# Performance work log

Measured on AMD Instinct MI355X. Metric: run time of the kernel, lower is better.

Reference implementation:

```python
import jax, jax.numpy as jnp
import numpy as np

EPS = 1e-5


def _lstm(x, W_ih, W_hh, b_ih, b_hh):
    # x: [B, T, in]; torch LSTM gate order i, f, g, o. Returns (last h, last c).
    def step(carry, xt):
        h, c = carry
        z = xt @ W_ih.T + h @ W_hh.T + (b_ih + b_hh)  # [B, 4H]
        i, f, g, o = jnp.split(z, 4, axis=-1)
        c = jax.nn.sigmoid(f) * c + jax.nn.sigmoid(i) * jnp.tanh(g)
        h = jax.nn.sigmoid(o) * jnp.tanh(c)
        return (h, c), None
    h0 = jnp.zeros((x.shape[0], W_hh.shape[1]), x.dtype)
    (h, c), _ = jax.lax.scan(step, (h0, h0), jnp.swapaxes(x, 0, 1))
    return h, c


def _bn_train(x, g, b):
    # BatchNorm1d in training mode: batch stats, biased variance.
    m = x.mean(axis=0)
    v = x.var(axis=0)
    return g * (x - m) * jax.lax.rsqrt(v + EPS) + b


def _forward(agent_traj, neighbours, aW_ih, aW_hh, ab_ih, ab_hh,
             nW_ih, nW_hh, nb_ih, nb_hh, dW_ih, dW_hh, db_ih, db_hh,
             pW, pb, rW, rb, m1W, m1b, g1, be1, m2W, m2b, g2, be2,
             i1W, i1b, ig1, ib1, i2W, i2b, ig2, ib2, segment_ids):
    B = agent_traj.shape[0]
    # relative distance: neighbour last position - owning agent's last position
    rel = neighbours[:, -1, :] - agent_traj[segment_ids, -1, :]          # [N, 2]
    agent_h, agent_c = _lstm(agent_traj, aW_ih, aW_hh, ab_ih, ab_hh)     # [B, 64]
    neigh_h, _ = _lstm(neighbours, nW_ih, nW_hh, nb_ih, nb_hh)           # [N, 64]
    rel_emb = rel @ rW.T + rb                                            # [N, 64]
    x = jnp.concatenate([neigh_h, rel_emb], axis=1)                      # [N, 128]
    x = _bn_train(jax.nn.relu(x @ m1W.T + m1b), g1, be1)                 # [N, 512]
    x = _bn_train(jax.nn.relu(x @ m2W.T + m2b), g2, be2)                 # [N, 1024]
    # per-sample max pooling over each sample's neighbours (zeros if none)
    pooled = jax.ops.segment_max(x, segment_ids, num_segments=B)         # [B, 1024]
    counts = jax.ops.segment_sum(jnp.ones((x.shape[0],), x.dtype), segment_ids, num_segments=B)
    pooled = jnp.where(counts[:, None] > 0, pooled, jnp.zeros((), x.dtype))
    d = jnp.concatenate([pooled, agent_h], axis=1)                       # [B, 1088]
    d = _bn_train(jax.nn.relu(d @ i1W.T + i1b), ig1, ib1)                # [B, 1024]
    d = _bn_train(jax.nn.relu(d @ i2W.T + i2b), ig2, ib2)                # [B, 64]

    def dec_step(carry, _):
        h, c = carry
        z = h @ dW_ih.T + h @ dW_hh.T + (db_ih + db_hh)
        i, f, g, o = jnp.split(z, 4, axis=-1)
        c = jax.nn.sigmoid(f) * c + jax.nn.sigmoid(i) * jnp.tanh(g)
        h = jax.nn.sigmoid(o) * jnp.tanh(c)
        return (h, c), h
    _, hs = jax.lax.scan(dec_step, (d, agent_c), None, length=30)        # [30, B, 64]
    pred = jnp.einsum('tbh,oh->bto', hs, pW) + pb                        # [B, 30, 2]
    return pred


def setup_inputs() -> dict:
    B, T, N, Tn, H = 2048, 20, 32768, 20, 64
    key = jax.random.key(0)
    ki = iter(jax.random.split(key, 40))
    def rn(shape, s=0.1):
        return jax.random.normal(next(ki), shape, dtype=jnp.float32) * s
    inp = dict(
        agent_traj=rn((B, T, 2), 1.0),
        neighbours=rn((N, Tn, 2), 1.0),
        aW_ih=rn((4 * H, 2)), aW_hh=rn((4 * H, H)), ab_ih=rn((4 * H,)), ab_hh=rn((4 * H,)),
        nW_ih=rn((4 * H, 2)), nW_hh=rn((4 * H, H)), nb_ih=rn((4 * H,)), nb_hh=rn((4 * H,)),
        dW_ih=rn((4 * H, H)), dW_hh=rn((4 * H, H)), db_ih=rn((4 * H,)), db_hh=rn((4 * H,)),
        pW=rn((2, H)), pb=rn((2,)),
        rW=rn((H, 2)), rb=rn((H,)),
        m1W=rn((512, 128)), m1b=rn((512,)),
        g1=jnp.ones((512,), jnp.float32), be1=jnp.zeros((512,), jnp.float32),
        m2W=rn((1024, 512)), m2b=rn((1024,)),
        g2=jnp.ones((1024,), jnp.float32), be2=jnp.zeros((1024,), jnp.float32),
        i1W=rn((1024, 1088)), i1b=rn((1024,)),
        ig1=jnp.ones((1024,), jnp.float32), ib1=jnp.zeros((1024,), jnp.float32),
        i2W=rn((H, 1024)), i2b=rn((H,)),
        ig2=jnp.ones((H,), jnp.float32), ib2=jnp.zeros((H,), jnp.float32),
        segment_ids=jnp.sort(jax.random.randint(next(ki), (N,), 0, B)).astype(jnp.int32),
    )
    return inp


def reference(agent_traj, neighbours, aW_ih, aW_hh, ab_ih, ab_hh,
              nW_ih, nW_hh, nb_ih, nb_hh, dW_ih, dW_hh, db_ih, db_hh,
              pW, pb, rW, rb, m1W, m1b, g1, be1, m2W, m2b, g2, be2,
              i1W, i1b, ig1, ib1, i2W, i2b, ig2, ib2, segment_ids):
    return _forward(agent_traj, neighbours, aW_ih, aW_hh, ab_ih, ab_hh,
                    nW_ih, nW_hh, nb_ih, nb_hh, dW_ih, dW_hh, db_ih, db_hh,
                    pW, pb, rW, rb, m1W, m1b, g1, be1, m2W, m2b, g2, be2,
                    i1W, i1b, ig1, ib1, i2W, i2b, ig2, ib2, segment_ids)
```

## Files before the change

kernel.cpp:

```cpp
#include <hip/hip_runtime.h>

#define EPS_BN 1e-5f

typedef __attribute__((ext_vector_type(8))) short short8;
typedef __attribute__((ext_vector_type(4))) float f32x4;

__device__ __forceinline__ float fast_rcp(float x) { return __builtin_amdgcn_rcpf(x); }
__device__ __forceinline__ float sigmoid_f(float x) { return fast_rcp(1.0f + __expf(-x)); }
__device__ __forceinline__ float tanh_f(float x) { return 1.0f - 2.0f * fast_rcp(__expf(2.0f * x) + 1.0f); }

__device__ __forceinline__ unsigned short f2bf(float f) {
    unsigned u = __float_as_uint(f);
    u += 0x7FFFu + ((u >> 16) & 1u);
    return (unsigned short)(u >> 16);
}
__device__ __forceinline__ unsigned pk_bf(float a, float b) {
    return (unsigned)f2bf(a) | ((unsigned)f2bf(b) << 16);
}
__device__ __forceinline__ float bf_hi(float f) {
    return __uint_as_float((unsigned)f2bf(f) << 16);
}

__device__ __forceinline__ void gload16(const unsigned short* g, unsigned short* l) {
    __builtin_amdgcn_global_load_lds(
        (const __attribute__((address_space(1))) unsigned int*)g,
        (__attribute__((address_space(3))) unsigned int*)l,
        16, 0, 0);
}

union AFrag { short e[8]; short8 v; };
union BFrag { uint4 u; short8 v; };

__global__ __launch_bounds__(256) void lstm_mfma(
    const float* __restrict__ xA,
    const float* __restrict__ aW_ih, const float* __restrict__ aW_hh,
    const float* __restrict__ ab_ih, const float* __restrict__ ab_hh,
    float* __restrict__ agent_h, float* __restrict__ agent_c,
    const float* __restrict__ xN,
    const float* __restrict__ nW_ih, const float* __restrict__ nW_hh,
    const float* __restrict__ nb_ih, const float* __restrict__ nb_hh,
    const int* __restrict__ seg, const float* __restrict__ rW,
    const float* __restrict__ rb,
    unsigned short* __restrict__ x0hi, unsigned short* __restrict__ x0lo,
    int nAgentBlk, int T)
{
    __shared__ unsigned h_ex[2][2][32 * 52];

    const bool isA = (blockIdx.x < (unsigned)nAgentBlk);
    const long blk = isA ? blockIdx.x : blockIdx.x - nAgentBlk;
    const float* __restrict__ x     = isA ? xA   : xN;
    const float* __restrict__ W_ih  = isA ? aW_ih : nW_ih;
    const float* __restrict__ W_hh  = isA ? aW_hh : nW_hh;
    const float* __restrict__ b_ih  = isA ? ab_ih : nb_ih;
    const float* __restrict__ b_hh  = isA ? ab_hh : nb_hh;

    const int tid  = threadIdx.x;
    const int w    = tid >> 6;
    const int lane = tid & 63;
    const int s    = lane & 15;
    const int q    = lane >> 4;

    short8 ahi[4][3], alo[4][3];
#pragma unroll
    for (int gt = 0; gt < 4; ++gt) {
        const int n = gt * 64 + w * 16 + s;
#pragma unroll
        for (int kc = 0; kc < 2; ++kc) {
            const float* src = &W_hh[n * 64 + kc * 32 + q * 8];
            float4 v0 = *(const float4*)src;
            float4 v1 = *(const float4*)(src + 4);
            float v[8] = {v0.x, v0.y, v0.z, v0.w, v1.x, v1.y, v1.z, v1.w};
            AFrag a, b;
#pragma unroll
            for (int j = 0; j < 8; ++j) {
                a.e[j] = (short)f2bf(v[j]);
                b.e[j] = (short)f2bf(v[j] - bf_hi(v[j]));
            }
            ahi[gt][kc] = a.v;
            alo[gt][kc] = b.v;
        }
        AFrag a2, b2;
#pragma unroll
        for (int j = 0; j < 8; ++j) { a2.e[j] = 0; b2.e[j] = 0; }
        if (q == 0) {
            const float wi0 = W_ih[n * 2 + 0];
            const float wi1 = W_ih[n * 2 + 1];
            const float bs  = b_ih[n] + b_hh[n];
            a2.e[0] = (short)f2bf(wi0); b2.e[0] = (short)f2bf(wi0 - bf_hi(wi0));
            a2.e[1] = (short)f2bf(wi1); b2.e[1] = (short)f2bf(wi1 - bf_hi(wi1));
            a2.e[2] = (short)f2bf(bs);  b2.e[2] = (short)f2bf(bs  - bf_hi(bs));
        }
        ahi[gt][2] = a2.v;
        alo[gt][2] = b2.v;
    }

    for (int i = tid; i < 2 * 2 * 32 * 52; i += 256) (&h_ex[0][0][0])[i] = 0u;
    __syncthreads();
    if (tid < 32) {
        h_ex[0][0][tid * 52 + 33] = pk_bf(1.0f, 0.0f);
        h_ex[1][0][tid * 52 + 33] = pk_bf(1.0f, 0.0f);
        float2 xv = *(const float2*)&x[(blk * 32 + tid) * (long)(T * 2)];
        h_ex[0][0][tid * 52 + 32] = pk_bf(xv.x, xv.y);
        h_ex[0][1][tid * 52 + 32] = pk_bf(xv.x - bf_hi(xv.x), xv.y - bf_hi(xv.y));
    }
    __syncthreads();

    float creg[2][4] = {{0.f, 0.f, 0.f, 0.f}, {0.f, 0.f, 0.f, 0.f}};

    for (int t = 0; t < T; ++t) {
        const int rb_ = t & 1, wb = rb_ ^ 1;
        BFrag bhi[2][3], blo[2][3];
#pragma unroll
        for (int g = 0; g < 2; ++g)
#pragma unroll
        for (int kc = 0; kc < 3; ++kc) {
            const int off = (g * 16 + s) * 52 + kc * 16 + (q >> 1) * 8 + (q & 1) * 4;
            bhi[g][kc].u = *(const uint4*)&h_ex[rb_][0][off];
            blo[g][kc].u = *(const uint4*)&h_ex[rb_][1][off];
        }

        f32x4 acc[4][2];
#pragma unroll
        for (int gt = 0; gt < 4; ++gt) { acc[gt][0] = (f32x4)0.f; acc[gt][1] = (f32x4)0.f; }

#pragma unroll
        for (int kc = 0; kc < 3; ++kc) {
#pragma unroll
            for (int g = 0; g < 2; ++g) {
                const short8 bh = bhi[g][kc].v;
                const short8 bl = blo[g][kc].v;
#pragma unroll
                for (int gt = 0; gt < 4; ++gt) {
                    f32x4 a = acc[gt][g];
                    a = __builtin_amdgcn_mfma_f32_16x16x32_bf16(ahi[gt][kc], bh, a, 0, 0, 0);
                    a = __builtin_amdgcn_mfma_f32_16x16x32_bf16(ahi[gt][kc], bl, a, 0, 0, 0);
                    a = __builtin_amdgcn_mfma_f32_16x16x32_bf16(alo[gt][kc], bh, a, 0, 0, 0);
                    acc[gt][g] = a;
                }
            }
        }

#pragma unroll
        for (int g = 0; g < 2; ++g) {
            float hval[4];
#pragma unroll
            for (int r = 0; r < 4; ++r) {
                const float ei = __expf(-acc[0][g][r]);
                const float eg = __expf(2.0f * acc[2][g][r]);
                const float it = (eg - 1.0f) * fast_rcp((1.0f + ei) * (eg + 1.0f));
                const float sf = fast_rcp(1.0f + __expf(-acc[1][g][r]));
                const float c  = fmaf(sf, creg[g][r], it);
                creg[g][r] = c;
                const float eo = __expf(-acc[3][g][r]);
                const float ec = __expf(2.0f * c);
                hval[r] = (ec - 1.0f) * fast_rcp((1.0f + eo) * (ec + 1.0f));
            }
            {
                const int w0 = (g * 16 + s) * 52 + w * 8 + q * 2;
                h_ex[wb][0][w0]     = pk_bf(hval[0], hval[1]);
                h_ex[wb][0][w0 + 1] = pk_bf(hval[2], hval[3]);
                h_ex[wb][1][w0]     = pk_bf(hval[0] - bf_hi(hval[0]), hval[1] - bf_hi(hval[1]));
                h_ex[wb][1][w0 + 1] = pk_bf(hval[2] - bf_hi(hval[2]), hval[3] - bf_hi(hval[3]));
            }
            if (t == T - 1) {
                const long seq = blk * 32 + g * 16 + s;
                const int j0 = w * 16 + q * 4;
                if (isA) {
                    *(float4*)&agent_h[seq * 64 + j0] =
                        make_float4(hval[0], hval[1], hval[2], hval[3]);
                    *(float4*)&agent_c[seq * 64 + j0] =
                        make_float4(creg[g][0], creg[g][1], creg[g][2], creg[g][3]);
                } else {
                    *(uint2*)&x0hi[seq * 128 + j0] = make_uint2(
                        pk_bf(hval[0], hval[1]), pk_bf(hval[2], hval[3]));
                    *(uint2*)&x0lo[seq * 128 + j0] = make_uint2(
                        pk_bf(hval[0] - bf_hi(hval[0]), hval[1] - bf_hi(hval[1])),
                        pk_bf(hval[2] - bf_hi(hval[2]), hval[3] - bf_hi(hval[3])));
                }
            }
        }
        if (tid < 32 && t + 1 < T) {
            float2 xv = *(const float2*)&x[(blk * 32 + tid) * (long)(T * 2) + (t + 1) * 2];
            h_ex[wb][0][tid * 52 + 32] = pk_bf(xv.x, xv.y);
            h_ex[wb][1][tid * 52 + 32] = pk_bf(xv.x - bf_hi(xv.x), xv.y - bf_hi(xv.y));
        }
        __syncthreads();
    }

    if (!isA) {
        const int sloc = tid >> 3;
        const long n = blk * 32 + sloc;
        const float2 np = *(const float2*)&x[n * (long)(T * 2) + (T - 1) * 2];
        const int sid = seg[n];
        const float2 ap = *(const float2*)&xA[(long)sid * (T * 2) + (T - 1) * 2];
        const float ra = np.x - ap.x, rbv = np.y - ap.y;
        const int o0 = (tid & 7) * 8;
#pragma unroll
        for (int j = 0; j < 8; ++j) {
            const int o = o0 + j;
            const float v = fmaf(rW[o * 2 + 0], ra, fmaf(rW[o * 2 + 1], rbv, rb[o]));
            x0hi[n * 128 + 64 + o] = f2bf(v);
            x0lo[n * 128 + 64 + o] = f2bf(v - bf_hi(v));
        }
    }
}

__device__ __forceinline__ void wfrag_body(
    const float* __restrict__ W, int K, int blk, int l,
    unsigned short* __restrict__ Whi, unsigned short* __restrict__ Wlo)
{
    const int nKc = K >> 5;
    const int ti = blk / nKc, kc = blk - ti * nKc;
    const int n = ti * 16 + (l & 15);
    const int k0 = kc * 32 + (l >> 4) * 8;
    const long ob = ((long)blk * 64 + l) * 8;
#pragma unroll
    for (int j = 0; j < 8; ++j) {
        float v = W[(long)n * K + k0 + j];
        Whi[ob + j] = f2bf(v);
        Wlo[ob + j] = f2bf(v - bf_hi(v));
    }
}

__global__ __launch_bounds__(64) void prep_all(
    const float* __restrict__ m1W, const float* __restrict__ m1b,
    const float* __restrict__ i1W, const float* __restrict__ i1b,
    const float* __restrict__ dW_ih, const float* __restrict__ dW_hh,
    const float* __restrict__ db_ih, const float* __restrict__ db_hh,
    unsigned short* __restrict__ W1hi, unsigned short* __restrict__ W1lo,
    float* __restrict__ b1f,
    unsigned short* __restrict__ Wi1hi, unsigned short* __restrict__ Wi1lo,
    float* __restrict__ bi1f,
    float* __restrict__ Wc, float* __restrict__ bc,
    float* __restrict__ accAll, float* __restrict__ poolraw)
{
    const int b = blockIdx.x, l = threadIdx.x;
    if (b < 128) {
        wfrag_body(m1W, 128, b, l, W1hi, W1lo);
    } else if (b < 2304) {
        wfrag_body(i1W, 1088, b - 128, l, Wi1hi, Wi1lo);
    } else if (b < 2312) {
        const int i = (b - 2304) * 64 + l;
        b1f[i] = m1b[i];
    } else if (b < 2328) {
        const int i = (b - 2312) * 64 + l;
        bi1f[i] = i1b[i];
    } else if (b < 2588) {
        const int idx = (b - 2328) * 64 + l;
        if (idx < 16384) Wc[idx] = dW_ih[idx] + dW_hh[idx];
        else if (idx < 16640) bc[idx - 16384] = db_ih[idx - 16384] + db_hh[idx - 16384];
    } else if (b < 2594) {
        const int i0 = (b - 2588) * 1024 + l;
#pragma unroll
        for (int j = 0; j < 16; ++j) {
            const int i = i0 + j * 64;
            if (i < 5248) accAll[i] = 0.f;
        }
    } else {
        const long i0 = (long)(b - 2594) * 1024 + l * 4;
        const float4 z = make_float4(0.f, 0.f, 0.f, 0.f);
#pragma unroll
        for (int j = 0; j < 4; ++j)
            *(float4*)&poolraw[i0 + j * 256] = z;
    }
}

__global__ __launch_bounds__(64) void prep_w2(
    const float* __restrict__ W,
    const float* __restrict__ b2,
    const float* __restrict__ acc1,
    const float* __restrict__ g1, const float* __restrict__ be1,
    float invN,
    unsigned short* __restrict__ Whi, unsigned short* __restrict__ Wlo,
    float* __restrict__ bout)
{
    const int K = 512, nKc = 16;
    const int blk = blockIdx.x, l = threadIdx.x;
    if (blk < 1024) {
        const int ti = blk / nKc, kc = blk - ti * nKc;
        const int n = ti * 16 + (l & 15);
        const int k0 = kc * 32 + (l >> 4) * 8;
        const long ob = ((long)blk * 64 + l) * 8;
#pragma unroll
        for (int j = 0; j < 8; ++j) {
            const int k = k0 + j;
            const float mean = acc1[k] * invN;
            const float var  = acc1[512 + k] * invN - mean * mean;
            const float sc   = g1[k] * rsqrtf(var + EPS_BN);
            const float v = W[(long)n * K + k] * sc;
            Whi[ob + j] = f2bf(v);
            Wlo[ob + j] = f2bf(v - bf_hi(v));
        }
    } else {
        const int n = blk - 1024;
        float s = 0.f;
        for (int k = l; k < K; k += 64) {
            const float mean = acc1[k] * invN;
            const float var  = acc1[512 + k] * invN - mean * mean;
            const float sc   = g1[k] * rsqrtf(var + EPS_BN);
            const float sh   = be1[k] - mean * sc;
            s += sh * W[(long)n * K + k];
        }
#pragma unroll
        for (int m = 32; m >= 1; m >>= 1) s += __shfl_xor(s, m, 64);
        if (l == 0) bout[n] = b2[n] + s;
    }
}

__global__ __launch_bounds__(256, 2) void gemm_split(
    const unsigned short* __restrict__ Ahi,
    const unsigned short* __restrict__ Alo,
    const unsigned short* __restrict__ Whi,
    const unsigned short* __restrict__ Wlo,
    const float* __restrict__ bias,
    float* __restrict__ Yf,
    unsigned short* __restrict__ Yhi,
    unsigned short* __restrict__ Ylo,
    float* __restrict__ accum,
    const int* __restrict__ segp,
    float* __restrict__ poolmax,
    int M, int K, int O)
{
    __shared__ unsigned short As[2][2][128 * 32];
    __shared__ int segl[128];
    const int t = threadIdx.x;
    const int lane = t & 63;
    const int w = t >> 6;
    const int wm = w & 1, wn = w >> 1;

    const int nx = gridDim.x;
    const int flat = blockIdx.y * nx + blockIdx.x;
    const int grp = flat / (8 * nx);
    const int loc = flat - grp * (8 * nx);
    const int m0 = (grp * 8 + (loc & 7)) * 128;
    const int n0 = (loc >> 3) * 128;
    const int nKc = K >> 5;

    f32x4 acc[4][4];
#pragma unroll
    for (int mt = 0; mt < 4; ++mt)
#pragma unroll
    for (int nt = 0; nt < 4; ++nt) acc[mt][nt] = (f32x4)0.f;

    const int rloc0 = w * 32 + (lane >> 2);
    const int rloc1 = rloc0 + 16;
    const int sd = lane & 3;
    const unsigned short* gsrc[2][2];
    gsrc[0][0] = Ahi + (long)(m0 + rloc0) * K + (sd ^ ((rloc0 >> 1) & 3)) * 8;
    gsrc[0][1] = Ahi + (long)(m0 + rloc1) * K + (sd ^ ((rloc1 >> 1) & 3)) * 8;
    gsrc[1][0] = Alo + (long)(m0 + rloc0) * K + (sd ^ ((rloc0 >> 1) & 3)) * 8;
    gsrc[1][1] = Alo + (long)(m0 + rloc1) * K + (sd ^ ((rloc1 >> 1) & 3)) * 8;

    auto stageA = [&](int buf, int kc) {
#pragma unroll
        for (int pp = 0; pp < 2; ++pp)
#pragma unroll
        for (int cc = 0; cc < 2; ++cc)
            gload16(gsrc[pp][cc] + kc * 32,
                    &As[buf][pp][(w * 32 + cc * 16) * 32]);
    };

    const int s2 = ((lane >> 4) ^ ((lane >> 1) & 3)) * 8;
    const int arow = wm * 64 + (lane & 15);
    const long bt0 = (long)((n0 >> 4) + wn * 4);

    auto loadB = [&](BFrag* bh, BFrag* bl, int kc) {
#pragma unroll
        for (int nt = 0; nt < 4; ++nt) {
            const long fb = ((bt0 + nt) * nKc + kc) * 512 + lane * 8;
            bh[nt].u = *(const uint4*)(Whi + fb);
            bl[nt].u = *(const uint4*)(Wlo + fb);
        }
    };
    auto compute = [&](int buf, BFrag* bh, BFrag* bl) {
        BFrag afh[4], afl[4];
#pragma unroll
        for (int mt = 0; mt < 4; ++mt) {
            afh[mt].u = *(const uint4*)&As[buf][0][(arow + mt * 16) * 32 + s2];
            afl[mt].u = *(const uint4*)&As[buf][1][(arow + mt * 16) * 32 + s2];
        }
#pragma unroll
        for (int nt = 0; nt < 4; ++nt)
#pragma unroll
        for (int mt = 0; mt < 4; ++mt) {
            f32x4 a = acc[mt][nt];
            a = __builtin_amdgcn_mfma_f32_16x16x32_bf16(afh[mt].v, bh[nt].v, a, 0, 0, 0);
            a = __builtin_amdgcn_mfma_f32_16x16x32_bf16(afh[mt].v, bl[nt].v, a, 0, 0, 0);
            a = __builtin_amdgcn_mfma_f32_16x16x32_bf16(afl[mt].v, bh[nt].v, a, 0, 0, 0);
            acc[mt][nt] = a;
        }
    };

    BFrag bh0[4], bl0[4], bh1[4], bl1[4];
    stageA(0, 0);
    loadB(bh0, bl0, 0);
    __syncthreads();
    for (int kc = 0; kc < nKc; kc += 2) {
        stageA(1, kc + 1);
        loadB(bh1, bl1, kc + 1);
        compute(0, bh0, bl0);
        __syncthreads();
        if (kc + 2 < nKc) {
            stageA(0, kc + 2);
            loadB(bh0, bl0, kc + 2);
        }
        compute(1, bh1, bl1);
        if (kc + 2 < nKc) __syncthreads();
    }

    int sid0 = 0, span = 0;
    bool useLds = false;
    float* pool = nullptr;
    if (segp) {
        __syncthreads();
        if (t < 128) segl[t] = segp[m0 + t];
        __syncthreads();
        sid0 = segl[0];
        span = segl[127] - sid0 + 1;
        pool = (float*)&As[0][0][0];
        useLds = (span <= 60);
        if (useLds) {
            for (int i = t; i < span * 132; i += 256) pool[i] = 0.f;
            __syncthreads();
        }
    }

    const int cn = lane & 15, cq = lane >> 4;
#pragma unroll
    for (int nt = 0; nt < 4; ++nt) {
        const int cl = wn * 64 + nt * 16 + cn;
        const int n = n0 + cl;
        const float bs = bias[n];
        float s = 0.f, ssq = 0.f;
#pragma unroll
        for (int mt = 0; mt < 4; ++mt) {
            const int mb = wm * 64 + mt * 16 + cq * 4;
            float vmax = 0.f; int sid = -1;
#pragma unroll
            for (int r = 0; r < 4; ++r) {
                const float v = fmaxf(acc[mt][nt][r] + bs, 0.f);
                s += v; ssq += v * v;
                if (segp) {
                    const int sr = segl[mb + r];
                    if (r == 0) { vmax = v; sid = sr; }
                    else if (sr == sid) { vmax = fmaxf(vmax, v); }
                    else {
                        if (vmax > 0.f) {
                            if (useLds)
                                atomicMax((int*)&pool[(sid - sid0) * 132 + cl], __float_as_int(vmax));
                            else
                                atomicMax((int*)&poolmax[(long)sid * O + n], __float_as_int(vmax));
                        }
                        sid = sr; vmax = v;
                    }
                } else if (Yf) {
                    Yf[(long)(m0 + mb + r) * O + n] = v;
                } else {
                    const long idx = (long)(m0 + mb + r) * O + n;
                    Yhi[idx] = f2bf(v);
                    Ylo[idx] = f2bf(v - bf_hi(v));
                }
            }
            if (segp && vmax > 0.f) {
                if (useLds)
                    atomicMax((int*)&pool[(sid - sid0) * 132 + cl], __float_as_int(vmax));
                else
                    atomicMax((int*)&poolmax[(long)sid * O + n], __float_as_int(vmax));
            }
        }
        if (accum) {
            s   += __shfl_xor(s, 16, 64);   ssq += __shfl_xor(ssq, 16, 64);
            s   += __shfl_xor(s, 32, 64);   ssq += __shfl_xor(ssq, 32, 64);
            if (cq == 0) {
                atomicAdd(&accum[n], s);
                atomicAdd(&accum[O + n], ssq);
            }
        }
    }

    if (segp && useLds) {
        __syncthreads();
        for (int e = t; e < span * 128; e += 256) {
            const int sl = e >> 7, c = e & 127;
            const float v = pool[sl * 132 + c];
            const long gi = (long)(sid0 + sl) * O + (n0 + c);
            if (sl == 0 || sl == span - 1) {
                if (v > 0.f) atomicMax((int*)&poolmax[gi], __float_as_int(v));
            } else {
                poolmax[gi] = v;
            }
        }
    }
}

__global__ __launch_bounds__(256) void bn_finalize(
    const float* __restrict__ accum, const float* __restrict__ g,
    const float* __restrict__ be, int O, float invM,
    float* __restrict__ scale, float* __restrict__ shift)
{
    const int o = blockIdx.x * 256 + threadIdx.x;
    if (o < O) {
        const float mean = accum[o] * invM;
        const float var  = accum[O + o] * invM - mean * mean;
        const float sc   = g[o] * rsqrtf(var + EPS_BN);
        scale[o] = sc;
        shift[o] = be[o] - mean * sc;
    }
}

__global__ __launch_bounds__(256) void build_d0(
    const float* __restrict__ poolraw, const float* __restrict__ agent_h,
    const int* __restrict__ seg, int N,
    const float* __restrict__ acc2, const float* __restrict__ g2,
    const float* __restrict__ be2, float invN,
    unsigned short* __restrict__ d0hi, unsigned short* __restrict__ d0lo)
{
    const int b = blockIdx.x;
    int l = 0, h = N;
    while (l < h) { const int mid = (l + h) >> 1; if (seg[mid] < b) l = mid + 1; else h = mid; }
    const bool nonempty = (l < N) && (seg[l] == b);
    for (int c = threadIdx.x; c < 1088; c += 256) {
        float v;
        if (c < 1024) {
            const float mean = acc2[c] * invN;
            const float var  = acc2[1024 + c] * invN - mean * mean;
            const float sc   = g2[c] * rsqrtf(var + EPS_BN);
            const float sh   = be2[c] - mean * sc;
            v = nonempty ? fmaf(sc, poolraw[(long)b * 1024 + c], sh) : 0.f;
        } else {
            v = agent_h[(long)b * 64 + (c - 1024)];
        }
        d0hi[(long)b * 1088 + c] = f2bf(v);
        d0lo[(long)b * 1088 + c] = f2bf(v - bf_hi(v));
    }
}

__global__ __launch_bounds__(256) void gemm_i2_part(
    const float* __restrict__ A,
    const float* __restrict__ W,
    const float* __restrict__ ascale, const float* __restrict__ ashift,
    float* __restrict__ part, int M, int K, int kchunk)
{
    __shared__ float As[16][132];
    __shared__ float Bs[16][68];
    const int t = threadIdx.x;
    const int m0 = blockIdx.x * 128;
    const int ks = blockIdx.y;
    const int kbeg = ks * kchunk;
    const int kend = kbeg + kchunk;
    const int tm = (t & 15) * 8;
    const int tn = (t >> 4) * 4;
    const int ar = t >> 1;
    const int ac = (t & 1) * 8;
    const int br = t >> 2;
    const int bc = (t & 3) * 4;

    float acc[8][4];
#pragma unroll
    for (int i = 0; i < 8; ++i)
#pragma unroll
    for (int j = 0; j < 4; ++j) acc[i][j] = 0.f;

    for (int k0 = kbeg; k0 < kend; k0 += 16) {
        float4 a0 = *(const float4*)&A[(long)(m0+ar)*K + k0 + ac];
        float4 a1 = *(const float4*)&A[(long)(m0+ar)*K + k0 + ac + 4];
        float4 s0 = *(const float4*)&ascale[k0 + ac];
        float4 s1 = *(const float4*)&ascale[k0 + ac + 4];
        float4 h0 = *(const float4*)&ashift[k0 + ac];
        float4 h1 = *(const float4*)&ashift[k0 + ac + 4];
        a0.x = fmaf(a0.x, s0.x, h0.x); a0.y = fmaf(a0.y, s0.y, h0.y);
        a0.z = fmaf(a0.z, s0.z, h0.z); a0.w = fmaf(a0.w, s0.w, h0.w);
        a1.x = fmaf(a1.x, s1.x, h1.x); a1.y = fmaf(a1.y, s1.y, h1.y);
        a1.z = fmaf(a1.z, s1.z, h1.z); a1.w = fmaf(a1.w, s1.w, h1.w);
        float4 b0 = *(const float4*)&W[(long)br*K + k0 + bc];
        __syncthreads();
        As[ac+0][ar] = a0.x; As[ac+1][ar] = a0.y; As[ac+2][ar] = a0.z; As[ac+3][ar] = a0.w;
        As[ac+4][ar] = a1.x; As[ac+5][ar] = a1.y; As[ac+6][ar] = a1.z; As[ac+7][ar] = a1.w;
        Bs[bc+0][br] = b0.x; Bs[bc+1][br] = b0.y; Bs[bc+2][br] = b0.z; Bs[bc+3][br] = b0.w;
        __syncthreads();
#pragma unroll
        for (int kk = 0; kk < 16; ++kk) {
            float av[8], bv[4];
            *(float4*)&av[0] = *(const float4*)&As[kk][tm];
            *(float4*)&av[4] = *(const float4*)&As[kk][tm + 4];
            *(float4*)&bv[0] = *(const float4*)&Bs[kk][tn];
#pragma unroll
            for (int i = 0; i < 8; ++i)
#pragma unroll
            for (int j = 0; j < 4; ++j)
                acc[i][j] = fmaf(av[i], bv[j], acc[i][j]);
        }
    }

    float* po = part + (long)ks * M * 64;
#pragma unroll
    for (int i = 0; i < 8; ++i)
        *(float4*)&po[(long)(m0 + tm + i) * 64 + tn] = *(float4*)&acc[i][0];
}

__global__ __launch_bounds__(256) void i2_finish_stats(
    const float* __restrict__ part, const float* __restrict__ bias,
    int M, int KS, float* __restrict__ t2, float* __restrict__ accum)
{
    __shared__ float l1[256], l2[256];
    const int t = threadIdx.x;
    const long base = (long)blockIdx.x * 2048;
    float s = 0.f, ss = 0.f;
#pragma unroll
    for (int k = 0; k < 8; ++k) {
        const long idx = base + k * 256 + t;
        float v = 0.f;
        for (int ks = 0; ks < KS; ++ks) v += part[(long)ks * M * 64 + idx];
        v = fmaxf(v + bias[idx & 63], 0.f);
        t2[idx] = v;
        s += v; ss += v * v;
    }
    l1[t] = s; l2[t] = ss;
    __syncthreads();
    if (t < 64) {
        s  = l1[t] + l1[t + 64] + l1[t + 128] + l1[t + 192];
        ss = l2[t] + l2[t + 64] + l2[t + 128] + l2[t + 192];
        atomicAdd(&accum[t], s);
        atomicAdd(&accum[64 + t], ss);
    }
}

__global__ __launch_bounds__(256) void decoder_kernel(
    const float* __restrict__ t2, const float* __restrict__ acc4,
    const float* __restrict__ ig2, const float* __restrict__ ib2, float invB,
    const float* __restrict__ agent_c,
    const float* __restrict__ Wc, const float* __restrict__ bc,
    const float* __restrict__ pW, const float* __restrict__ pb,
    float* __restrict__ pred )
{
    __shared__ float h_lds[2][64];
    __shared__ float zg_lds[2][64];
    __shared__ float zo_lds[2][64];
    const int t = threadIdx.x;
    const int lane = t & 63;
    const int wave = t >> 6;
    const int s = wave >> 1;
    const int role = wave & 1;
    const long seq = (long)blockIdx.x * 2 + s;

    const int r0 = role * 128 + lane;
    const int r1 = r0 + 64;
    float w0[64], w1[64];
#pragma unroll
    for (int k = 0; k < 64; k += 4) {
        float4 va = *(const float4*)&Wc[r0 * 64 + k];
        w0[k] = va.x; w0[k+1] = va.y; w0[k+2] = va.z; w0[k+3] = va.w;
        float4 vb = *(const float4*)&Wc[r1 * 64 + k];
        w1[k] = vb.x; w1[k+1] = vb.y; w1[k+2] = vb.z; w1[k+3] = vb.w;
    }
    const float bias0 = bc[r0];
    const float bias1 = bc[r1];
    const float pw0 = pW[lane], pw1 = pW[64 + lane];
    const float pb0 = pb[0], pb1 = pb[1];

    float c = agent_c[seq*64 + lane];
    if (role == 0) {
        const float mean = acc4[lane] * invB;
        const float var  = acc4[64 + lane] * invB - mean * mean;
        const float sc   = ig2[lane] * rsqrtf(var + EPS_BN);
        const float sh   = ib2[lane] - mean * sc;
        h_lds[s][lane] = fmaf(sc, t2[seq*64 + lane], sh);
    }
    __syncthreads();
    float hv = h_lds[s][lane];

    for (int step = 0; step < 30; ++step) {
        float z0 = bias0, z1 = bias1;
#pragma unroll
        for (int k = 0; k < 64; ++k) {
            float hk = __int_as_float(__builtin_amdgcn_readlane(__float_as_int(hv), k));
            z0 = fmaf(hk, w0[k], z0);
            z1 = fmaf(hk, w1[k], z1);
        }
        if (role == 1) { zg_lds[s][lane] = z0; zo_lds[s][lane] = z1; }
        __syncthreads();
        if (role == 0) {
            const float ig = sigmoid_f(z0);
            const float fg = sigmoid_f(z1);
            const float gg = tanh_f(zg_lds[s][lane]);
            const float og = sigmoid_f(zo_lds[s][lane]);
            c = fmaf(fg, c, ig * gg);
            h_lds[s][lane] = og * tanh_f(c);
        }
        __syncthreads();
        hv = h_lds[s][lane];
        if (role == 0) {
            float p0 = hv * pw0;
            float p1 = hv * pw1;
#pragma unroll
            for (int m = 32; m >= 1; m >>= 1) {
                p0 += __shfl_xor(p0, m, 64);
                p1 += __shfl_xor(p1, m, 64);
            }
            if (lane == 0) {
                pred[seq*60 + step*2 + 0] = p0 + pb0;
                pred[seq*60 + step*2 + 1] = p1 + pb1;
            }
        }
    }
}

extern "C" void kernel_launch(void* const* d_in, const int* in_sizes, int n_in,
                              void* d_out, int out_size, void* d_ws, size_t ws_size,
                              hipStream_t stream)
{
    const float* agent_traj = (const float*)d_in[0];
    const float* neighbours = (const float*)d_in[1];
    const float* aW_ih = (const float*)d_in[2];
    const float* aW_hh = (const float*)d_in[3];
    const float* ab_ih = (const float*)d_in[4];
    const float* ab_hh = (const float*)d_in[5];
    const float* nW_ih = (const float*)d_in[6];
    const float* nW_hh = (const float*)d_in[7];
    const float* nb_ih = (const float*)d_in[8];
    const float* nb_hh = (const float*)d_in[9];
    const float* dW_ih = (const float*)d_in[10];
    const float* dW_hh = (const float*)d_in[11];
    const float* db_ih = (const float*)d_in[12];
    const float* db_hh = (const float*)d_in[13];
    const float* pW = (const float*)d_in[14];
    const float* pb = (const float*)d_in[15];
    const float* rW = (const float*)d_in[16];
    const float* rb = (const float*)d_in[17];
    const float* m1W = (const float*)d_in[18];
    const float* m1b = (const float*)d_in[19];
    const float* g1  = (const float*)d_in[20];
    const float* be1 = (const float*)d_in[21];
    const float* m2W = (const float*)d_in[22];
    const float* m2b = (const float*)d_in[23];
    const float* g2  = (const float*)d_in[24];
    const float* be2 = (const float*)d_in[25];
    const float* i1W = (const float*)d_in[26];
    const float* i1b = (const float*)d_in[27];
    const float* ig1 = (const float*)d_in[28];
    const float* ib1 = (const float*)d_in[29];
    const float* i2W = (const float*)d_in[30];
    const float* i2b = (const float*)d_in[31];
    const float* ig2 = (const float*)d_in[32];
    const float* ib2 = (const float*)d_in[33];
    const int*   seg = (const int*)d_in[34];
    float* pred = (float*)d_out;

    const int B = 2048, T = 20, N = 32768;

    char* p = (char*)d_ws;
    auto alloc = [&](size_t bytes) -> char* {
        char* r = p; p += (bytes + 255) & ~(size_t)255; return r;
    };
    float* agent_h = (float*)alloc((size_t)B*64*4);
    float* agent_c = (float*)alloc((size_t)B*64*4);
    char* neigh_region = alloc((size_t)N*64*4);
    unsigned short* x0hi = (unsigned short*)alloc((size_t)N*128*2);
    unsigned short* x0lo = (unsigned short*)alloc((size_t)N*128*2);
    char* y1hi_region  = alloc((size_t)N*512*2);
    unsigned short* y1lo = (unsigned short*)alloc((size_t)N*512*2);
    float* poolraw = (float*)alloc((size_t)B*1024*4);
    float* accAll = (float*)alloc((size_t)(1024+2048+2048+128)*4);
    float* acc1 = accAll;
    float* acc2 = accAll + 1024;
    float* acc3 = accAll + 3072;
    float* acc4 = accAll + 5120;
    float* sc3 = (float*)alloc(1024*4); float* sh3 = (float*)alloc(1024*4);
    float* Wc = (float*)alloc(256*64*4);
    float* bc = (float*)alloc(256*4);
    unsigned short* W1hi = (unsigned short*)alloc((size_t)512*128*2);
    unsigned short* W1lo = (unsigned short*)alloc((size_t)512*128*2);
    unsigned short* W2hi = (unsigned short*)alloc((size_t)1024*512*2);
    unsigned short* W2lo = (unsigned short*)alloc((size_t)1024*512*2);
    unsigned short* Wi1hi = (unsigned short*)alloc((size_t)1024*1088*2);
    unsigned short* Wi1lo = (unsigned short*)alloc((size_t)1024*1088*2);
    float* b1f = (float*)alloc(512*4);
    float* b2f = (float*)alloc(1024*4);
    float* bi1f = (float*)alloc(1024*4);
    float* i2part = (float*)alloc((size_t)8*B*64*4);

    float* t1 = (float*)neigh_region;
    unsigned short* y1hi = (unsigned short*)y1hi_region;
    unsigned short* d0hi = (unsigned short*)y1hi_region;
    unsigned short* d0lo = d0hi + (size_t)B*1088;
    float* t2 = (float*)(y1hi_region + (size_t)2*B*1088*2);

    prep_all<<<4642, 64, 0, stream>>>(m1W, m1b, i1W, i1b, dW_ih, dW_hh, db_ih, db_hh,
                                      W1hi, W1lo, b1f, Wi1hi, Wi1lo, bi1f, Wc, bc,
                                      accAll, poolraw);

    lstm_mfma<<<B/32 + N/32, 256, 0, stream>>>(
        agent_traj, aW_ih, aW_hh, ab_ih, ab_hh, agent_h, agent_c,
        neighbours, nW_ih, nW_hh, nb_ih, nb_hh,
        seg, rW, rb, x0hi, x0lo, B/32, T);

    gemm_split<<<dim3(512/128, N/128), 256, 0, stream>>>(
        x0hi, x0lo, W1hi, W1lo, b1f, nullptr, y1hi, y1lo, acc1,
        nullptr, nullptr, N, 128, 512);

    prep_w2<<<2048, 64, 0, stream>>>(m2W, m2b, acc1, g1, be1, 1.0f/N,
                                     W2hi, W2lo, b2f);

    gemm_split<<<dim3(1024/128, N/128), 256, 0, stream>>>(
        y1hi, y1lo, W2hi, W2lo, b2f, nullptr, nullptr, nullptr, acc2,
        seg, poolraw, N, 512, 1024);

    build_d0<<<B, 256, 0, stream>>>(poolraw, agent_h, seg, N, acc2, g2, be2,
                                    1.0f/N, d0hi, d0lo);

    gemm_split<<<dim3(1024/128, B/128), 256, 0, stream>>>(
        d0hi, d0lo, Wi1hi, Wi1lo, bi1f, t1, nullptr, nullptr, acc3,
        nullptr, nullptr, B, 1088, 1024);
    bn_finalize<<<4, 256, 0, stream>>>(acc3, ig1, ib1, 1024, 1.0f/B, sc3, sh3);

    gemm_i2_part<<<dim3(B/128, 8), 256, 0, stream>>>(t1, i2W, sc3, sh3, i2part,
                                                     B, 1024, 128);
    i2_finish_stats<<<64, 256, 0, stream>>>(i2part, i2b, B, 8, t2, acc4);

    decoder_kernel<<<B/2, 256, 0, stream>>>(t2, acc4, ig2, ib2, 1.0f/B,
                                            agent_c, Wc, bc, pW, pb, pred);
}
```

Before: 581.9 us.

## Stage 64-wide K chunks of A in LDS to halve barriers in split GEMM

The A tile staged in shared memory grows from 32 to 64 K-columns per buffer, using a new XOR swizzle, and each loop iteration now computes two 32-wide sub-chunks from one buffer. This halves the number of __syncthreads per K step and issues larger async global-to-LDS loads, which should cut synchronization stalls in the hi/lo bf16 MFMA GEMM. In exchange the kernel uses twice the LDS (64 KB for A), which may lower occupancy below the requested two blocks per SM. The larger buffer also lets the LDS pooling path handle spans up to 120 segments.

```diff
diff --git a/kernel.cpp b/kernel.cpp
--- a/kernel.cpp
+++ b/kernel.cpp
@@ -321,7 +321,7 @@
     float* __restrict__ poolmax,
     int M, int K, int O)
 {
-    __shared__ unsigned short As[2][2][128 * 32];
+    __shared__ unsigned short As[2][2][128 * 64];
     __shared__ int segl[128];
     const int t = threadIdx.x;
     const int lane = t & 63;
@@ -342,25 +342,24 @@
 #pragma unroll
     for (int nt = 0; nt < 4; ++nt) acc[mt][nt] = (f32x4)0.f;
 
-    const int rloc0 = w * 32 + (lane >> 2);
-    const int rloc1 = rloc0 + 16;
-    const int sd = lane & 3;
-    const unsigned short* gsrc[2][2];
-    gsrc[0][0] = Ahi + (long)(m0 + rloc0) * K + (sd ^ ((rloc0 >> 1) & 3)) * 8;
-    gsrc[0][1] = Ahi + (long)(m0 + rloc1) * K + (sd ^ ((rloc1 >> 1) & 3)) * 8;
-    gsrc[1][0] = Alo + (long)(m0 + rloc0) * K + (sd ^ ((rloc0 >> 1) & 3)) * 8;
-    gsrc[1][1] = Alo + (long)(m0 + rloc1) * K + (sd ^ ((rloc1 >> 1) & 3)) * 8;
-
-    auto stageA = [&](int buf, int kc) {
+    const int rl = w * 32 + (lane >> 3);
+    const int sl = (lane & 7) ^ (lane >> 3);
+    const long gcol = (long)((sl >> 2) * 32 + (sl & 3) * 8);
+    const unsigned short* gA[2];
+    gA[0] = Ahi + (long)(m0 + rl) * K + gcol;
+    gA[1] = Alo + (long)(m0 + rl) * K + gcol;
+
+    auto stageA = [&](int buf, int kc2) {
 #pragma unroll
         for (int pp = 0; pp < 2; ++pp)
 #pragma unroll
-        for (int cc = 0; cc < 2; ++cc)
-            gload16(gsrc[pp][cc] + kc * 32,
-                    &As[buf][pp][(w * 32 + cc * 16) * 32]);
+        for (int cc = 0; cc < 4; ++cc)
+            gload16(gA[pp] + (long)cc * 8 * K + kc2 * 32,
+                    &As[buf][pp][(w * 32 + cc * 8) * 64]);
     };
 
-    const int s2 = ((lane >> 4) ^ ((lane >> 1) & 3)) * 8;
+    const int s2a = (((lane >> 4) + 0) ^ (lane & 7)) * 8;
+    const int s2b = (((lane >> 4) + 4) ^ (lane & 7)) * 8;
     const int arow = wm * 64 + (lane & 15);
     const long bt0 = (long)((n0 >> 4) + wn * 4);
 
@@ -372,12 +371,12 @@
             bl[nt].u = *(const uint4*)(Wlo + fb);
         }
     };
-    auto compute = [&](int buf, BFrag* bh, BFrag* bl) {
+    auto compute = [&](int buf, int s2, BFrag* bh, BFrag* bl) {
         BFrag afh[4], afl[4];
 #pragma unroll
         for (int mt = 0; mt < 4; ++mt) {
-            afh[mt].u = *(const uint4*)&As[buf][0][(arow + mt * 16) * 32 + s2];
-            afl[mt].u = *(const uint4*)&As[buf][1][(arow + mt * 16) * 32 + s2];
+            afh[mt].u = *(const uint4*)&As[buf][0][(arow + mt * 16) * 64 + s2];
+            afl[mt].u = *(const uint4*)&As[buf][1][(arow + mt * 16) * 64 + s2];
         }
 #pragma unroll
         for (int nt = 0; nt < 4; ++nt)
@@ -395,17 +394,15 @@
     stageA(0, 0);
     loadB(bh0, bl0, 0);
     __syncthreads();
-    for (int kc = 0; kc < nKc; kc += 2) {
-        stageA(1, kc + 1);
-        loadB(bh1, bl1, kc + 1);
-        compute(0, bh0, bl0);
-        __syncthreads();
-        if (kc + 2 < nKc) {
-            stageA(0, kc + 2);
-            loadB(bh0, bl0, kc + 2);
-        }
-        compute(1, bh1, bl1);
-        if (kc + 2 < nKc) __syncthreads();
+    int buf = 0;
+    for (int kc2 = 0; kc2 < nKc; kc2 += 2) {
+        if (kc2 + 2 < nKc) stageA(buf ^ 1, kc2 + 2);
+        loadB(bh1, bl1, kc2 + 1);
+        compute(buf, s2a, bh0, bl0);
+        if (kc2 + 2 < nKc) loadB(bh0, bl0, kc2 + 2);
+        compute(buf, s2b, bh1, bl1);
+        if (kc2 + 2 < nKc) __syncthreads();
+        buf ^= 1;
     }
 
     int sid0 = 0, span = 0;
@@ -418,7 +415,7 @@
         sid0 = segl[0];
         span = segl[127] - sid0 + 1;
         pool = (float*)&As[0][0][0];
-        useLds = (span <= 60);
+        useLds = (span <= 120);
         if (useLds) {
             for (int i = t; i < span * 132; i += 256) pool[i] = 0.f;
             __syncthreads();
@@ -481,10 +478,10 @@
     if (segp && useLds) {
         __syncthreads();
         for (int e = t; e < span * 128; e += 256) {
-            const int sl = e >> 7, c = e & 127;
-            const float v = pool[sl * 132 + c];
-            const long gi = (long)(sid0 + sl) * O + (n0 + c);
-            if (sl == 0 || sl == span - 1) {
+            const int sl_ = e >> 7, c = e & 127;
+            const float v = pool[sl_ * 132 + c];
+            const long gi = (long)(sid0 + sl_) * O + (n0 + c);
+            if (sl_ == 0 || sl_ == span - 1) {
                 if (v > 0.f) atomicMax((int*)&poolmax[gi], __float_as_int(v));
             } else {
                 poolmax[gi] = v;
```

New measurement: 572.5 us. No clear change (-1.6%).
